# Kernel tuning notes

Hardware: AMD Instinct MI355X
Metric: run time of the kernel (lower is better)

The kernel has to match this reference:

```python
import jax, jax.numpy as jnp
import numpy as np

NUM_NODES = 20000
HIDDEN = 64
NUM_EDGES = 640000
LEAK = 0.2  # PyG GATConv negative_slope default


def gat_conv(x, w, a_src, a_dst, b, src, dst, n):
    # x: [N, F_in]; w: [F_in, H*C]; a_src/a_dst: [H, C]; edges j=src -> i=dst
    H, C = a_src.shape
    xe = (x @ w).reshape(n, H, C)                         # [N, H, C]
    es = jnp.einsum('nhc,hc->nh', xe, a_src)              # alpha_src per node
    ed = jnp.einsum('nhc,hc->nh', xe, a_dst)              # alpha_dst per node
    e = jax.nn.leaky_relu(es[src] + ed[dst], LEAK)        # [E, H] edge logits
    # segment softmax over each destination's incoming edges
    m = jax.ops.segment_max(e, dst, num_segments=n)
    p = jnp.exp(e - m[dst])
    s = jax.ops.segment_sum(p, dst, num_segments=n)
    alpha = p / s[dst]                                    # [E, H]
    out = jax.ops.segment_sum(alpha[:, :, None] * xe[src], dst, num_segments=n)
    return out.reshape(n, H * C) + b                      # concat heads + bias


def setup_inputs() -> dict:
    key = jax.random.key(0)
    ks = jax.random.split(key, 16)
    B, S, N, Hd = 4, 12, NUM_NODES, HIDDEN
    sc = 0.1
    inp = {}
    inp['x'] = jax.random.normal(ks[0], (B, S, N), jnp.float32)
    inp['edge_index'] = jax.random.randint(ks[1], (2, NUM_EDGES), 0, N, jnp.int32)
    inp['proj_w'] = jax.random.normal(ks[2], (S, Hd), jnp.float32) * sc
    inp['proj_b'] = jnp.zeros((Hd,), jnp.float32)
    inp['gat0_w'] = jax.random.normal(ks[3], (Hd, Hd), jnp.float32) * sc
    inp['gat0_asrc'] = jax.random.normal(ks[4], (8, 8), jnp.float32) * sc
    inp['gat0_adst'] = jax.random.normal(ks[5], (8, 8), jnp.float32) * sc
    inp['gat0_b'] = jnp.zeros((Hd,), jnp.float32)
    inp['gat1_w'] = jax.random.normal(ks[6], (Hd, Hd), jnp.float32) * sc
    inp['gat1_asrc'] = jax.random.normal(ks[7], (8, 8), jnp.float32) * sc
    inp['gat1_adst'] = jax.random.normal(ks[8], (8, 8), jnp.float32) * sc
    inp['gat1_b'] = jnp.zeros((Hd,), jnp.float32)
    inp['gat2_w'] = jax.random.normal(ks[9], (Hd, Hd), jnp.float32) * sc
    inp['gat2_asrc'] = jax.random.normal(ks[10], (1, Hd), jnp.float32) * sc
    inp['gat2_adst'] = jax.random.normal(ks[11], (1, Hd), jnp.float32) * sc
    inp['gat2_b'] = jnp.zeros((Hd,), jnp.float32)
    inp['conv_w'] = jax.random.normal(ks[12], (Hd, Hd, 3), jnp.float32) * sc
    inp['conv_b'] = jnp.zeros((Hd,), jnp.float32)
    inp['out_w'] = jax.random.normal(ks[13], (Hd, 3), jnp.float32) * sc
    inp['out_b'] = jnp.zeros((3,), jnp.float32)
    return inp


def reference(x, edge_index, proj_w, proj_b,
              gat0_w, gat0_asrc, gat0_adst, gat0_b,
              gat1_w, gat1_asrc, gat1_adst, gat1_b,
              gat2_w, gat2_asrc, gat2_adst, gat2_b,
              conv_w, conv_b, out_w, out_b):
    B, S, N = x.shape
    # PyG GATConv add_self_loops=True
    loops = jnp.arange(N, dtype=edge_index.dtype)
    src = jnp.concatenate([edge_index[0], loops])
    dst = jnp.concatenate([edge_index[1], loops])
    h = jnp.transpose(x, (0, 2, 1)) @ proj_w + proj_b     # [B, N, Hd]
    layers = [(gat0_w, gat0_asrc, gat0_adst, gat0_b),
              (gat1_w, gat1_asrc, gat1_adst, gat1_b),
              (gat2_w, gat2_asrc, gat2_adst, gat2_b)]
    for i, (w, asr, ads, b) in enumerate(layers):
        h = jax.vmap(lambda hb: gat_conv(hb, w, asr, ads, b, src, dst, N))(h)
        if i < len(layers) - 1:
            h = jax.nn.elu(h)                             # dropout is identity in eval
    hc = jnp.transpose(h, (0, 2, 1))                      # [B, Hd, N]
    hc = jax.lax.conv_general_dilated(hc, conv_w, (1,), ((1, 1),),
                                      dimension_numbers=('NCH', 'OIH', 'NCH'))
    hc = jax.nn.relu(hc + conv_b[None, :, None])
    h = jnp.transpose(hc, (0, 2, 1)) @ out_w + out_b      # [B, N, pred]
    return jnp.transpose(h, (0, 2, 1))                    # [B, pred, N]
```

## Files before the change

### kernel.cpp

```cpp
#include <hip/hip_runtime.h>
#include <math.h>

constexpr int B  = 4;
constexpr int S  = 12;
constexpr int N  = 20000;
constexpr int HD = 64;
constexpr int E0 = 640000;
constexpr int EL = E0 + N;
constexpr int BN = B * N;
constexpr int CAP = 128;

__global__ void scatter_kernel(const int* __restrict__ ei, int* __restrict__ cnt,
                               int* __restrict__ perm) {
    int e = blockIdx.x * blockDim.x + threadIdx.x;
    if (e >= EL) return;
    int s, d;
    if (e < E0) { s = ei[e]; d = ei[E0 + e]; }
    else        { s = e - E0; d = s; }
    int pos = atomicAdd(&cnt[d], 1) & (CAP - 1);
    perm[d * CAP + pos] = s;
}

__global__ void tw_kernel(const float* __restrict__ cw, float* __restrict__ cwD) {
    int i = blockIdx.x * blockDim.x + threadIdx.x;
    if (i >= HD * HD * 3) return;
    int o = i / (HD * 3), rem = i % (HD * 3), c = rem / 3, dt = rem % 3;
    cwD[dt * (HD * HD) + c * HD + o] = cw[i];
}

constexpr int GT = 64;

template<int H>
__global__ __launch_bounds__(256, 4)
void gemm_attn_kernel(const float* __restrict__ hin, const float* __restrict__ w,
                      const float* __restrict__ asrc, const float* __restrict__ adst,
                      float* __restrict__ xe, float* __restrict__ es, float* __restrict__ ed) {
    __shared__ float tile[GT * HD];
    int base = blockIdx.x * GT;
    for (int i = threadIdx.x; i < GT * (HD / 4); i += 256)
        ((float4*)tile)[i] = ((const float4*)(hin + (size_t)base * HD))[i];
    int lane = threadIdx.x & 63;
    float wres[HD];
    #pragma unroll
    for (int c = 0; c < HD; ++c) wres[c] = w[c * HD + lane];
    float as_ = asrc[lane], ad_ = adst[lane];
    __syncthreads();
    int wvid = threadIdx.x >> 6;
    for (int j = wvid * 16; j < wvid * 16 + 16; ++j) {
        int t = base + j;
        float acc = 0.f;
        #pragma unroll
        for (int cq = 0; cq < 16; ++cq) {
            float4 r = ((const float4*)tile)[j * 16 + cq];
            acc = fmaf(r.x, wres[4 * cq + 0], acc);
            acc = fmaf(r.y, wres[4 * cq + 1], acc);
            acc = fmaf(r.z, wres[4 * cq + 2], acc);
            acc = fmaf(r.w, wres[4 * cq + 3], acc);
        }
        xe[(size_t)t * HD + lane] = acc;
        float t0 = acc * as_, t1 = acc * ad_;
        if (H == 8) {
            #pragma unroll
            for (int m = 1; m < 8; m <<= 1) {
                t0 += __shfl_xor(t0, m, 64);
                t1 += __shfl_xor(t1, m, 64);
            }
            if ((lane & 7) == 0) {
                es[t * 8 + (lane >> 3)] = t0;
                ed[t * 8 + (lane >> 3)] = t1;
            }
        } else {
            #pragma unroll
            for (int m = 1; m < 64; m <<= 1) {
                t0 += __shfl_xor(t0, m, 64);
                t1 += __shfl_xor(t1, m, 64);
            }
            if (lane == 0) { es[t] = t0; ed[t] = t1; }
        }
    }
}

__global__ __launch_bounds__(256, 4)
void fused0_kernel(const float* __restrict__ x, const float* __restrict__ pw,
                   const float* __restrict__ pb, const float* __restrict__ w,
                   const float* __restrict__ asrc, const float* __restrict__ adst,
                   float* __restrict__ xe, float* __restrict__ es, float* __restrict__ ed) {
    __shared__ float tile[GT * HD];
    __shared__ float xt[S * GT];
    int base = blockIdx.x * GT;
    for (int i = threadIdx.x; i < S * GT; i += 256) {
        int s = i >> 6, nl = i & 63;
        int t = base + nl, bb = t / N, n = t - bb * N;
        xt[i] = x[(bb * S + s) * N + n];
    }
    int lane = threadIdx.x & 63;
    float wres[HD];
    #pragma unroll
    for (int c = 0; c < HD; ++c) wres[c] = w[c * HD + lane];
    float pwres[S];
    #pragma unroll
    for (int s = 0; s < S; ++s) pwres[s] = pw[s * HD + lane];
    float pbv = pb[lane];
    float as_ = asrc[lane], ad_ = adst[lane];
    __syncthreads();
    int wvid = threadIdx.x >> 6;
    for (int j = wvid * 16; j < wvid * 16 + 16; ++j) {
        float hl = pbv;
        #pragma unroll
        for (int s = 0; s < S; ++s)
            hl = fmaf(xt[s * GT + j], pwres[s], hl);
        tile[j * HD + lane] = hl;
    }
    for (int j = wvid * 16; j < wvid * 16 + 16; ++j) {
        int t = base + j;
        float acc = 0.f;
        #pragma unroll
        for (int cq = 0; cq < 16; ++cq) {
            float4 r = ((const float4*)tile)[j * 16 + cq];
            acc = fmaf(r.x, wres[4 * cq + 0], acc);
            acc = fmaf(r.y, wres[4 * cq + 1], acc);
            acc = fmaf(r.z, wres[4 * cq + 2], acc);
            acc = fmaf(r.w, wres[4 * cq + 3], acc);
        }
        xe[(size_t)t * HD + lane] = acc;
        float t0 = acc * as_, t1 = acc * ad_;
        #pragma unroll
        for (int m = 1; m < 8; m <<= 1) {
            t0 += __shfl_xor(t0, m, 64);
            t1 += __shfl_xor(t1, m, 64);
        }
        if ((lane & 7) == 0) {
            es[t * 8 + (lane >> 3)] = t0;
            ed[t * 8 + (lane >> 3)] = t1;
        }
    }
}

template<int H, bool DO_ELU>
__global__ __launch_bounds__(256, 8)
void agg_kernel(const float* __restrict__ xe, const float* __restrict__ es,
                const float* __restrict__ ed, const int* __restrict__ cnt,
                const int* __restrict__ perm, const float* __restrict__ bias,
                float* __restrict__ hout) {
    int g = blockIdx.x;
    int bb   = (g & 7) >> 1;
    int idx  = (g >> 3) * 2 + (g & 1);
    int node = idx * 4 + (threadIdx.x >> 6);
    int lane  = threadIdx.x & 63;
    int group = lane >> 4;
    int c4    = lane & 15;
    int deg = cnt[node];
    int baseE = node * CAP;
    int h = (H == 8) ? (c4 >> 1) : 0;
    const float*  es_b = es + bb * (N * H);
    const float4* xe4  = (const float4*)(xe + bb * (N * HD));
    float edv = ed[(bb * N + node) * H + h];
    float4 acc = {0.f, 0.f, 0.f, 0.f};
    float ssum = 0.f;
    #pragma unroll 4
    for (int jb = 0; jb < deg; jb += 4) {
        int j = jb + group;
        bool valid = (j < deg);
        int src = perm[baseE + (valid ? j : 0)];
        float e = es_b[src * H + h] + edv;
        e = fmaxf(e, 0.2f * e);
        float p = valid ? __expf(e) : 0.f;
        ssum += p;
        float4 xv = xe4[src * 16 + c4];
        acc.x = fmaf(p, xv.x, acc.x);
        acc.y = fmaf(p, xv.y, acc.y);
        acc.z = fmaf(p, xv.z, acc.z);
        acc.w = fmaf(p, xv.w, acc.w);
    }
    #pragma unroll
    for (int m = 16; m < 64; m <<= 1) {
        acc.x += __shfl_xor(acc.x, m, 64);
        acc.y += __shfl_xor(acc.y, m, 64);
        acc.z += __shfl_xor(acc.z, m, 64);
        acc.w += __shfl_xor(acc.w, m, 64);
        ssum  += __shfl_xor(ssum,  m, 64);
    }
    if (lane < 16) {
        float inv = 1.f / ssum;
        const float4* b4 = (const float4*)bias;
        float4 bv = b4[c4];
        float4 r;
        r.x = acc.x * inv + bv.x;
        r.y = acc.y * inv + bv.y;
        r.z = acc.z * inv + bv.z;
        r.w = acc.w * inv + bv.w;
        if (DO_ELU) {
            r.x = (r.x > 0.f) ? r.x : expm1f(r.x);
            r.y = (r.y > 0.f) ? r.y : expm1f(r.y);
            r.z = (r.z > 0.f) ? r.z : expm1f(r.z);
            r.w = (r.w > 0.f) ? r.w : expm1f(r.w);
        }
        ((float4*)hout)[(bb * N + node) * 16 + c4] = r;
    }
}

constexpr int CN = 64;
__global__ __launch_bounds__(256, 2)
void conv_out_kernel(const float* __restrict__ h, const float* __restrict__ cwD,
                     const float* __restrict__ cb, const float* __restrict__ ow,
                     const float* __restrict__ ob, float* __restrict__ out) {
    __shared__ float tile[(CN + 2) * HD];
    __shared__ float part[CN * HD];
    int bb = blockIdx.y;
    int base = blockIdx.x * CN;
    for (int i = threadIdx.x; i < (CN + 2) * (HD / 4); i += 256) {
        int row = i >> 4, q = i & 15;
        int m = base - 1 + row;
        float4 v = {0.f, 0.f, 0.f, 0.f};
        if (m >= 0 && m < N) v = ((const float4*)(h + ((size_t)bb * N + m) * HD))[q];
        ((float4*)tile)[i] = v;
    }
    int lane = threadIdx.x & 63;
    int wvid = threadIdx.x >> 6;
    float cbv = cb[lane];
    float ow0 = ow[lane * 3 + 0], ow1 = ow[lane * 3 + 1], ow2 = ow[lane * 3 + 2];
    float ob0 = ob[0], ob1 = ob[1], ob2 = ob[2];
    #pragma unroll
    for (int j = 0; j < 16; ++j)
        part[(wvid * 16 + j) * HD + lane] = cbv;
    __syncthreads();
    #pragma unroll 1
    for (int dt = 0; dt < 3; ++dt) {
        float wres[HD];
        #pragma unroll
        for (int c = 0; c < HD; ++c) wres[c] = cwD[dt * (HD * HD) + c * HD + lane];
        #pragma unroll 1
        for (int j = 0; j < 16; ++j) {
            const float4* rp = (const float4*)(tile + (wvid * 16 + j + dt) * HD);
            float a = 0.f;
            #pragma unroll
            for (int cq = 0; cq < 16; ++cq) {
                float4 r = rp[cq];
                a = fmaf(r.x, wres[4 * cq + 0], a);
                a = fmaf(r.y, wres[4 * cq + 1], a);
                a = fmaf(r.z, wres[4 * cq + 2], a);
                a = fmaf(r.w, wres[4 * cq + 3], a);
            }
            part[(wvid * 16 + j) * HD + lane] += a;
        }
    }
    #pragma unroll 1
    for (int j = 0; j < 16; ++j) {
        float v = fmaxf(part[(wvid * 16 + j) * HD + lane], 0.f);
        float t0 = v * ow0, t1 = v * ow1, t2 = v * ow2;
        #pragma unroll
        for (int m = 1; m < 64; m <<= 1) {
            t0 += __shfl_xor(t0, m, 64);
            t1 += __shfl_xor(t1, m, 64);
            t2 += __shfl_xor(t2, m, 64);
        }
        int n = base + wvid * 16 + j;
        if (lane < 3 && n < N) {
            float r = (lane == 0) ? t0 + ob0 : (lane == 1) ? t1 + ob1 : t2 + ob2;
            out[(size_t)bb * 3 * N + lane * N + n] = r;
        }
    }
}

extern "C" void kernel_launch(void* const* d_in, const int* in_sizes, int n_in,
                              void* d_out, int out_size, void* d_ws, size_t ws_size,
                              hipStream_t stream) {
    const float* x      = (const float*)d_in[0];
    const int*   ei     = (const int*)  d_in[1];
    const float* proj_w = (const float*)d_in[2];
    const float* proj_b = (const float*)d_in[3];
    const float* g_w [3] = {(const float*)d_in[4], (const float*)d_in[8],  (const float*)d_in[12]};
    const float* g_as[3] = {(const float*)d_in[5], (const float*)d_in[9],  (const float*)d_in[13]};
    const float* g_ad[3] = {(const float*)d_in[6], (const float*)d_in[10], (const float*)d_in[14]};
    const float* g_b [3] = {(const float*)d_in[7], (const float*)d_in[11], (const float*)d_in[15]};
    const float* conv_w = (const float*)d_in[16];
    const float* conv_b = (const float*)d_in[17];
    const float* out_w  = (const float*)d_in[18];
    const float* out_b  = (const float*)d_in[19];
    float* out = (float*)d_out;

    float* bufA = (float*)d_ws;
    float* bufX = bufA + (size_t)BN * HD;
    float* es   = bufX + (size_t)BN * HD;
    float* ed   = es   + (size_t)BN * 8;
    int* cnt  = (int*)(ed + (size_t)BN * 8);
    int* perm = cnt + N;
    float* cwD = (float*)(perm + (size_t)N * CAP);

    const int TB = 256;
    const int gE = (EL + TB - 1) / TB;

    hipMemsetAsync(cnt, 0, N * sizeof(int), stream);
    scatter_kernel<<<gE, TB, 0, stream>>>(ei, cnt, perm);

    tw_kernel<<<(HD * HD * 3 + TB - 1) / TB, TB, 0, stream>>>(conv_w, cwD);

    fused0_kernel<<<BN / GT, TB, 0, stream>>>(x, proj_w, proj_b, g_w[0], g_as[0], g_ad[0],
                                              bufX, es, ed);
    agg_kernel<8, true><<<BN / 4, TB, 0, stream>>>(bufX, es, ed, cnt, perm, g_b[0], bufA);

    gemm_attn_kernel<8><<<BN / GT, TB, 0, stream>>>(bufA, g_w[1], g_as[1], g_ad[1], bufX, es, ed);
    agg_kernel<8, true><<<BN / 4, TB, 0, stream>>>(bufX, es, ed, cnt, perm, g_b[1], bufA);

    gemm_attn_kernel<1><<<BN / GT, TB, 0, stream>>>(bufA, g_w[2], g_as[2], g_ad[2], bufX, es, ed);
    agg_kernel<1, false><<<BN / 4, TB, 0, stream>>>(bufX, es, ed, cnt, perm, g_b[2], bufA);

    conv_out_kernel<<<dim3((N + CN - 1) / CN, B), TB, 0, stream>>>(bufA, cwD, conv_b, out_w, out_b, out);
}
```

Baseline: 480.1 us.

## Shrink conv kernel to single-wave blocks reading rows directly from global

The conv+output kernel now uses one 64-thread wave per block covering 16 nodes instead of four waves covering 64 nodes. It drops the shared-memory staging tile and its barrier, and reads each input row directly from global memory, where all lanes load the same address so the read is a broadcast. The goal is more blocks and no block-wide synchronisation. In exchange, each row is fetched from global memory three times, once per tap, and the column weights held in registers are reloaded for every 16 nodes instead of every 64, which multiplies weight traffic.

```diff
diff --git a/kernel.cpp b/kernel.cpp
--- a/kernel.cpp
+++ b/kernel.cpp
@@ -199,54 +199,41 @@
     }
 }
 
-constexpr int CN = 64;
-__global__ __launch_bounds__(256, 2)
+constexpr int CVN = 16;
+__global__ __launch_bounds__(64, 2)
 void conv_out_kernel(const float* __restrict__ h, const float* __restrict__ cwD,
                      const float* __restrict__ cb, const float* __restrict__ ow,
                      const float* __restrict__ ob, float* __restrict__ out) {
-    __shared__ float tile[(CN + 2) * HD];
-    __shared__ float part[CN * HD];
+    __shared__ float part[CVN * HD];
     int bb = blockIdx.y;
-    int base = blockIdx.x * CN;
-    for (int i = threadIdx.x; i < (CN + 2) * (HD / 4); i += 256) {
-        int row = i >> 4, q = i & 15;
-        int m = base - 1 + row;
-        float4 v = {0.f, 0.f, 0.f, 0.f};
-        if (m >= 0 && m < N) v = ((const float4*)(h + ((size_t)bb * N + m) * HD))[q];
-        ((float4*)tile)[i] = v;
-    }
-    int lane = threadIdx.x & 63;
-    int wvid = threadIdx.x >> 6;
+    int base = blockIdx.x * CVN;
+    int lane = threadIdx.x;
     float cbv = cb[lane];
     float ow0 = ow[lane * 3 + 0], ow1 = ow[lane * 3 + 1], ow2 = ow[lane * 3 + 2];
     float ob0 = ob[0], ob1 = ob[1], ob2 = ob[2];
     #pragma unroll
-    for (int j = 0; j < 16; ++j)
-        part[(wvid * 16 + j) * HD + lane] = cbv;
-    __syncthreads();
+    for (int j = 0; j < CVN; ++j) part[j * HD + lane] = cbv;
     #pragma unroll 1
     for (int dt = 0; dt < 3; ++dt) {
         float wres[HD];
         #pragma unroll
         for (int c = 0; c < HD; ++c) wres[c] = cwD[dt * (HD * HD) + c * HD + lane];
         #pragma unroll 1
-        for (int j = 0; j < 16; ++j) {
-            const float4* rp = (const float4*)(tile + (wvid * 16 + j + dt) * HD);
-            float a = 0.f;
-            #pragma unroll
-            for (int cq = 0; cq < 16; ++cq) {
-                float4 r = rp[cq];
-                a = fmaf(r.x, wres[4 * cq + 0], a);
-                a = fmaf(r.y, wres[4 * cq + 1], a);
-                a = fmaf(r.z, wres[4 * cq + 2], a);
-                a = fmaf(r.w, wres[4 * cq + 3], a);
-            }
-            part[(wvid * 16 + j) * HD + lane] += a;
+        for (int j = 0; j < CVN; ++j) {
+            int m = base + j + dt - 1;
+            if (m >= 0 && m < N) {
+                const float* hp = h + ((size_t)bb * N + m) * HD;
+                float a = 0.f;
+                #pragma unroll
+                for (int c = 0; c < HD; ++c)
+                    a = fmaf(hp[c], wres[c], a);
+                part[j * HD + lane] += a;
+            }
         }
     }
     #pragma unroll 1
-    for (int j = 0; j < 16; ++j) {
-        float v = fmaxf(part[(wvid * 16 + j) * HD + lane], 0.f);
+    for (int j = 0; j < CVN; ++j) {
+        float v = fmaxf(part[j * HD + lane], 0.f);
         float t0 = v * ow0, t1 = v * ow1, t2 = v * ow2;
         #pragma unroll
         for (int m = 1; m < 64; m <<= 1) {
@@ -254,8 +241,8 @@
             t1 += __shfl_xor(t1, m, 64);
             t2 += __shfl_xor(t2, m, 64);
         }
-        int n = base + wvid * 16 + j;
-        if (lane < 3 && n < N) {
+        int n = base + j;
+        if (lane < 3) {
             float r = (lane == 0) ? t0 + ob0 : (lane == 1) ? t1 + ob1 : t2 + ob2;
             out[(size_t)bb * 3 * N + lane * N + n] = r;
         }
@@ -305,5 +292,5 @@
     gemm_attn_kernel<1><<<BN / GT, TB, 0, stream>>>(bufA, g_w[2], g_as[2], g_ad[2], bufX, es, ed);
     agg_kernel<1, false><<<BN / 4, TB, 0, stream>>>(bufX, es, ed, cnt, perm, g_b[2], bufA);
 
-    conv_out_kernel<<<dim3((N + CN - 1) / CN, B), TB, 0, stream>>>(bufA, cwD, conv_b, out_w, out_b, out);
-}
+    conv_out_kernel<<<dim3(N / CVN, B), 64, 0, stream>>>(bufA, cwD, conv_b, out_w, out_b, out);
+}
```

New measurement: 447.2 us. 6.9% less time.
